# Kernel optimization log

Measured on AMD Instinct MI355X. Metric: run time of the kernel, lower is better.

Reference implementation:

```python
import jax, jax.numpy as jnp
import numpy as np

N_CLASSES = 18

def setup_inputs() -> dict:
    key = jax.random.key(0)
    k1, k2 = jax.random.split(key)
    B = 2_000_000
    output = jax.random.normal(k1, (B, N_CLASSES), dtype=jnp.float32)
    labels_soft = jax.random.uniform(k2, (B, N_CLASSES), dtype=jnp.float32)
    return {"output": output, "labels_soft": labels_soft}

def reference(output, labels_soft):
    # Original: sum over classes of mean_b( CE(output, cls) * labels_soft[:, cls] )
    # = mean over batch of sum_c( -log_softmax(output)[b, c] * labels_soft[b, c] )
    logp = jax.nn.log_softmax(output, axis=-1)          # [B, C]
    per_row = -jnp.sum(logp * labels_soft, axis=-1)     # [B]
    return jnp.mean(per_row)
```

## Files before the change

kernel.cpp:

```cpp
#include <hip/hip_runtime.h>

#define NCLS   18
#define TROWS  128
#define TWORDS (TROWS * NCLS)
#define CHUNKS (TWORDS / 256)

#define AS1 __attribute__((address_space(1)))
#define AS3 __attribute__((address_space(3)))

__global__ __launch_bounds__(256) void ce_soft_main(
    const float* __restrict__ logits,
    const float* __restrict__ labels,
    float* __restrict__ partial,
    int B)
{
    __shared__ float sX[2][TWORDS];
    __shared__ float sL[2][TWORDS];
    __shared__ float sWS[4];

    const int tid  = threadIdx.x;
    const int lane = tid & 63;
    const int wid  = tid >> 6;
    const int p    = tid >> 1;
    const int h    = tid & 1;
    const int nTiles = B / TROWS;
    const int grid = gridDim.x;

    float acc = 0.0f;
    int cur = 0;

    int t0 = blockIdx.x;
    if (t0 < nTiles) {
        const float* gx = logits + (size_t)t0 * TWORDS;
        const float* gl = labels + (size_t)t0 * TWORDS;
        for (int c = wid; c < CHUNKS; c += 4) {
            __builtin_amdgcn_global_load_lds((const AS1 void*)(gx + c * 256 + lane * 4),
                                             (AS3 void*)(&sX[0][c * 256]), 16, 0, 0);
            __builtin_amdgcn_global_load_lds((const AS1 void*)(gl + c * 256 + lane * 4),
                                             (AS3 void*)(&sL[0][c * 256]), 16, 0, 0);
        }
    }

    for (int t = t0; t < nTiles; t += grid) {
        __syncthreads();

        int tn = t + grid;
        if (tn < nTiles) {
            const float* gx = logits + (size_t)tn * TWORDS;
            const float* gl = labels + (size_t)tn * TWORDS;
            float* dX = &sX[cur ^ 1][0];
            float* dL = &sL[cur ^ 1][0];
            for (int c = wid; c < CHUNKS; c += 4) {
                __builtin_amdgcn_global_load_lds((const AS1 void*)(gx + c * 256 + lane * 4),
                                                 (AS3 void*)(dX + c * 256), 16, 0, 0);
                __builtin_amdgcn_global_load_lds((const AS1 void*)(gl + c * 256 + lane * 4),
                                                 (AS3 void*)(dL + c * 256), 16, 0, 0);
            }
        }

        const float2* rx = (const float2*)(&sX[cur][p * NCLS]);
        const float2* rl = (const float2*)(&sL[cur][p * NCLS]);
        float2 xv[5], lv[5];
        const int n = 5 - h;
        #pragma unroll
        for (int k = 0; k < 5; ++k) {
            int c = 2 * k + h;
            if (k < n) { xv[k] = rx[c];                      lv[k] = rl[c]; }
            else       { xv[k] = make_float2(-1e30f, -1e30f); lv[k] = make_float2(0.f, 0.f); }
        }
        float m = xv[0].x;
        #pragma unroll
        for (int k = 0; k < 5; ++k) { m = fmaxf(m, xv[k].x); m = fmaxf(m, xv[k].y); }
        m = fmaxf(m, __shfl_xor(m, 1, 64));
        float se = 0.f, dot = 0.f, sl = 0.f;
        #pragma unroll
        for (int k = 0; k < 5; ++k) {
            se += __expf(xv[k].x - m) + __expf(xv[k].y - m);
            dot = fmaf(lv[k].x, xv[k].x, dot);
            dot = fmaf(lv[k].y, xv[k].y, dot);
            sl += lv[k].x + lv[k].y;
        }
        se += __shfl_xor(se, 1, 64);
        float lse = m + __logf(se);
        acc = fmaf(sl, lse, acc - dot);
        cur ^= 1;
    }

    for (int row = nTiles * TROWS + blockIdx.x * blockDim.x + tid; row < B;
         row += grid * blockDim.x) {
        const float2* o2 = (const float2*)(logits + (size_t)row * NCLS);
        const float2* l2 = (const float2*)(labels + (size_t)row * NCLS);
        float x[NCLS], l[NCLS];
        #pragma unroll
        for (int k = 0; k < NCLS / 2; ++k) {
            float2 v = o2[k]; x[2 * k] = v.x; x[2 * k + 1] = v.y;
            float2 w = l2[k]; l[2 * k] = w.x; l[2 * k + 1] = w.y;
        }
        float mm = x[0];
        #pragma unroll
        for (int c = 1; c < NCLS; ++c) mm = fmaxf(mm, x[c]);
        float se = 0.f, dot = 0.f, sl = 0.f;
        #pragma unroll
        for (int c = 0; c < NCLS; ++c) {
            se += __expf(x[c] - mm);
            dot = fmaf(l[c], x[c], dot);
            sl += l[c];
        }
        acc = fmaf(sl, mm + __logf(se), acc - dot);
    }

    #pragma unroll
    for (int off = 32; off > 0; off >>= 1)
        acc += __shfl_down(acc, off, 64);
    if (lane == 0) sWS[wid] = acc;
    __syncthreads();
    if (tid == 0)
        partial[blockIdx.x] = sWS[0] + sWS[1] + sWS[2] + sWS[3];
}

__global__ __launch_bounds__(256) void ce_soft_finish(
    const float* __restrict__ partial, float* __restrict__ result,
    int n, float invB)
{
    float s = 0.f;
    for (int i = threadIdx.x; i < n; i += 256) s += partial[i];
    #pragma unroll
    for (int off = 32; off > 0; off >>= 1)
        s += __shfl_down(s, off, 64);
    __shared__ float ws[4];
    int lane = threadIdx.x & 63, wid = threadIdx.x >> 6;
    if (lane == 0) ws[wid] = s;
    __syncthreads();
    if (threadIdx.x == 0)
        result[0] = (ws[0] + ws[1] + ws[2] + ws[3]) * invB;
}

extern "C" void kernel_launch(void* const* d_in, const int* in_sizes, int n_in,
                              void* d_out, int out_size, void* d_ws, size_t ws_size,
                              hipStream_t stream) {
    const float* logits = (const float*)d_in[0];
    const float* labels = (const float*)d_in[1];
    float* result = (float*)d_out;

    int B = in_sizes[0] / NCLS;

    int grid = 1024;
    size_t need = (size_t)grid * sizeof(float);
    if (ws_size < need) {
        grid = (int)(ws_size / sizeof(float));
        if (grid > 1024) grid = 1024;
        if (grid < 1) grid = 1;
    }
    float* partial = (float*)d_ws;

    ce_soft_main<<<grid, 256, 0, stream>>>(logits, labels, partial, B);
    ce_soft_finish<<<1, 256, 0, stream>>>(partial, result, grid, 1.0f / (float)B);
}
```

Before: 286.7 us.

## Give each wave its own tiles with register double-buffered prefetch through private LDS

Replaces the block-wide LDS double buffer, which used async global-to-LDS loads and a __syncthreads every tile, with a per-wave scheme. Each wave owns its own LDS slice and keeps two tiles of logits and labels in registers, so the next loads are issued before the current tile is computed. Each lane now handles two full rows from LDS, so the pairwise shuffles go away, and the dot product is folded into a single fma per element. The grid is halved to 512 blocks with launch_bounds(256,2). The cost is very high register pressure (four 9-float4 arrays) and larger LDS per block, which may limit occupancy or cause spills.

```diff
diff --git a/kernel.cpp b/kernel.cpp
--- a/kernel.cpp
+++ b/kernel.cpp
@@ -3,91 +3,115 @@
 #define NCLS   18
 #define TROWS  128
 #define TWORDS (TROWS * NCLS)
-#define CHUNKS (TWORDS / 256)
+#define NV4    9
 
-#define AS1 __attribute__((address_space(1)))
-#define AS3 __attribute__((address_space(3)))
+__device__ __forceinline__ void tile_body(
+    float4* __restrict__ bufX, float4* __restrict__ bufL, int lane,
+    float4 (&xr)[NV4], float4 (&lr)[NV4],
+    const float* __restrict__ logits, const float* __restrict__ labels,
+    int tn, int nTiles, float& acc)
+{
+    #pragma unroll
+    for (int j = 0; j < NV4; ++j) bufX[j * 64 + lane] = xr[j];
+    #pragma unroll
+    for (int j = 0; j < NV4; ++j) bufL[j * 64 + lane] = lr[j];
 
-__global__ __launch_bounds__(256) void ce_soft_main(
+    if (tn < nTiles) {
+        const float4* gx = (const float4*)(logits + (size_t)tn * TWORDS);
+        const float4* gl = (const float4*)(labels + (size_t)tn * TWORDS);
+        #pragma unroll
+        for (int j = 0; j < NV4; ++j) xr[j] = gx[j * 64 + lane];
+        #pragma unroll
+        for (int j = 0; j < NV4; ++j) lr[j] = gl[j * 64 + lane];
+    }
+
+    float x[2 * NCLS];
+    #pragma unroll
+    for (int j = 0; j < NV4; ++j) {
+        float4 v = bufX[lane * 9 + j];
+        x[4 * j + 0] = v.x; x[4 * j + 1] = v.y;
+        x[4 * j + 2] = v.z; x[4 * j + 3] = v.w;
+    }
+    float mA = x[0], mB = x[18];
+    #pragma unroll
+    for (int c = 1; c < NCLS; ++c) { mA = fmaxf(mA, x[c]); mB = fmaxf(mB, x[NCLS + c]); }
+    float seA = 0.f, seB = 0.f;
+    #pragma unroll
+    for (int c = 0; c < NCLS; ++c) {
+        seA += __expf(x[c] - mA);
+        seB += __expf(x[NCLS + c] - mB);
+    }
+    float lseA = mA + __logf(seA);
+    float lseB = mB + __logf(seB);
+
+    #pragma unroll
+    for (int j = 0; j < NV4; ++j) {
+        float4 w = bufL[lane * 9 + j];
+        float s0 = (4 * j + 0 < NCLS) ? lseA : lseB;
+        float s1 = (4 * j + 1 < NCLS) ? lseA : lseB;
+        float s2 = (4 * j + 2 < NCLS) ? lseA : lseB;
+        float s3 = (4 * j + 3 < NCLS) ? lseA : lseB;
+        acc = fmaf(w.x, s0 - x[4 * j + 0], acc);
+        acc = fmaf(w.y, s1 - x[4 * j + 1], acc);
+        acc = fmaf(w.z, s2 - x[4 * j + 2], acc);
+        acc = fmaf(w.w, s3 - x[4 * j + 3], acc);
+    }
+}
+
+__global__ __launch_bounds__(256, 2) void ce_soft_main(
     const float* __restrict__ logits,
     const float* __restrict__ labels,
     float* __restrict__ partial,
     int B)
 {
-    __shared__ float sX[2][TWORDS];
-    __shared__ float sL[2][TWORDS];
+    __shared__ float sX[4][TWORDS];
+    __shared__ float sL[4][TWORDS];
     __shared__ float sWS[4];
 
     const int tid  = threadIdx.x;
     const int lane = tid & 63;
     const int wid  = tid >> 6;
-    const int p    = tid >> 1;
-    const int h    = tid & 1;
-    const int nTiles = B / TROWS;
-    const int grid = gridDim.x;
+    float4* bufX = (float4*)sX[wid];
+    float4* bufL = (float4*)sL[wid];
 
-    float acc = 0.0f;
-    int cur = 0;
+    const int nTiles  = B / TROWS;
+    const int wgid    = blockIdx.x * 4 + wid;
+    const int wstride = gridDim.x * 4;
 
-    int t0 = blockIdx.x;
-    if (t0 < nTiles) {
-        const float* gx = logits + (size_t)t0 * TWORDS;
-        const float* gl = labels + (size_t)t0 * TWORDS;
-        for (int c = wid; c < CHUNKS; c += 4) {
-            __builtin_amdgcn_global_load_lds((const AS1 void*)(gx + c * 256 + lane * 4),
-                                             (AS3 void*)(&sX[0][c * 256]), 16, 0, 0);
-            __builtin_amdgcn_global_load_lds((const AS1 void*)(gl + c * 256 + lane * 4),
-                                             (AS3 void*)(&sL[0][c * 256]), 16, 0, 0);
+    float acc = 0.f;
+    float4 xA[NV4], lA[NV4], xB[NV4], lB[NV4];
+
+    {
+        int tA = wgid, tB = wgid + wstride;
+        if (tA < nTiles) {
+            const float4* gx = (const float4*)(logits + (size_t)tA * TWORDS);
+            const float4* gl = (const float4*)(labels + (size_t)tA * TWORDS);
+            #pragma unroll
+            for (int j = 0; j < NV4; ++j) xA[j] = gx[j * 64 + lane];
+            #pragma unroll
+            for (int j = 0; j < NV4; ++j) lA[j] = gl[j * 64 + lane];
+        }
+        if (tB < nTiles) {
+            const float4* gx = (const float4*)(logits + (size_t)tB * TWORDS);
+            const float4* gl = (const float4*)(labels + (size_t)tB * TWORDS);
+            #pragma unroll
+            for (int j = 0; j < NV4; ++j) xB[j] = gx[j * 64 + lane];
+            #pragma unroll
+            for (int j = 0; j < NV4; ++j) lB[j] = gl[j * 64 + lane];
         }
     }
 
-    for (int t = t0; t < nTiles; t += grid) {
-        __syncthreads();
-
-        int tn = t + grid;
-        if (tn < nTiles) {
-            const float* gx = logits + (size_t)tn * TWORDS;
-            const float* gl = labels + (size_t)tn * TWORDS;
-            float* dX = &sX[cur ^ 1][0];
-            float* dL = &sL[cur ^ 1][0];
-            for (int c = wid; c < CHUNKS; c += 4) {
-                __builtin_amdgcn_global_load_lds((const AS1 void*)(gx + c * 256 + lane * 4),
-                                                 (AS3 void*)(dX + c * 256), 16, 0, 0);
-                __builtin_amdgcn_global_load_lds((const AS1 void*)(gl + c * 256 + lane * 4),
-                                                 (AS3 void*)(dL + c * 256), 16, 0, 0);
-            }
-        }
-
-        const float2* rx = (const float2*)(&sX[cur][p * NCLS]);
-        const float2* rl = (const float2*)(&sL[cur][p * NCLS]);
-        float2 xv[5], lv[5];
-        const int n = 5 - h;
-        #pragma unroll
-        for (int k = 0; k < 5; ++k) {
-            int c = 2 * k + h;
-            if (k < n) { xv[k] = rx[c];                      lv[k] = rl[c]; }
-            else       { xv[k] = make_float2(-1e30f, -1e30f); lv[k] = make_float2(0.f, 0.f); }
-        }
-        float m = xv[0].x;
-        #pragma unroll
-        for (int k = 0; k < 5; ++k) { m = fmaxf(m, xv[k].x); m = fmaxf(m, xv[k].y); }
-        m = fmaxf(m, __shfl_xor(m, 1, 64));
-        float se = 0.f, dot = 0.f, sl = 0.f;
-        #pragma unroll
-        for (int k = 0; k < 5; ++k) {
-            se += __expf(xv[k].x - m) + __expf(xv[k].y - m);
-            dot = fmaf(lv[k].x, xv[k].x, dot);
-            dot = fmaf(lv[k].y, xv[k].y, dot);
-            sl += lv[k].x + lv[k].y;
-        }
-        se += __shfl_xor(se, 1, 64);
-        float lse = m + __logf(se);
-        acc = fmaf(sl, lse, acc - dot);
-        cur ^= 1;
+    for (int t = wgid; t < nTiles; t += 2 * wstride) {
+        tile_body(bufX, bufL, lane, xA, lA, logits, labels,
+                  t + 2 * wstride, nTiles, acc);
+        int t1 = t + wstride;
+        if (t1 < nTiles)
+            tile_body(bufX, bufL, lane, xB, lB, logits, labels,
+                      t1 + 2 * wstride, nTiles, acc);
     }
 
     for (int row = nTiles * TROWS + blockIdx.x * blockDim.x + tid; row < B;
-         row += grid * blockDim.x) {
+         row += gridDim.x * blockDim.x) {
         const float2* o2 = (const float2*)(logits + (size_t)row * NCLS);
         const float2* l2 = (const float2*)(labels + (size_t)row * NCLS);
         float x[NCLS], l[NCLS];
@@ -144,11 +168,10 @@
 
     int B = in_sizes[0] / NCLS;
 
-    int grid = 1024;
-    size_t need = (size_t)grid * sizeof(float);
-    if (ws_size < need) {
+    int grid = 512;
+    if (ws_size < (size_t)grid * sizeof(float)) {
         grid = (int)(ws_size / sizeof(float));
-        if (grid > 1024) grid = 1024;
+        if (grid > 512) grid = 512;
         if (grid < 1) grid = 1;
     }
     float* partial = (float*)d_ws;
```

Result: slower. 343.2 us (+19.7%).

## Switch to per-wave tiles with register prefetch and no block barriers

Applied to the files above, without the earlier changes.

Each wavefront now processes its own 128-row tile, prefetching the next tile into registers with float4 loads and staging through a private LDS buffer, with each lane computing two full rows. This removes block-wide __syncthreads and the pairwise lane shuffles of the previous layout. The grid size is halved. It trades the async global-to-LDS double buffer for higher register pressure and possible LDS bank conflicts from the 9-float4 row stride.

```diff
diff --git a/kernel.cpp b/kernel.cpp
--- a/kernel.cpp
+++ b/kernel.cpp
@@ -3,10 +3,9 @@
 #define NCLS   18
 #define TROWS  128
 #define TWORDS (TROWS * NCLS)
-#define CHUNKS (TWORDS / 256)
+#define NF4    (TWORDS / 4)
 
-#define AS1 __attribute__((address_space(1)))
-#define AS3 __attribute__((address_space(3)))
+#define REP9(F) F(0) F(1) F(2) F(3) F(4) F(5) F(6) F(7) F(8)
 
 __global__ __launch_bounds__(256) void ce_soft_main(
     const float* __restrict__ logits,
@@ -14,80 +13,116 @@
     float* __restrict__ partial,
     int B)
 {
-    __shared__ float sX[2][TWORDS];
-    __shared__ float sL[2][TWORDS];
+    __shared__ float4 sX[4][NF4];
+    __shared__ float4 sL[4][NF4];
     __shared__ float sWS[4];
 
     const int tid  = threadIdx.x;
     const int lane = tid & 63;
     const int wid  = tid >> 6;
-    const int p    = tid >> 1;
-    const int h    = tid & 1;
-    const int nTiles = B / TROWS;
-    const int grid = gridDim.x;
+    float4* bufX = &sX[wid][0];
+    float4* bufL = &sL[wid][0];
+
+    const int nTiles  = B / TROWS;
+    const int wgid    = blockIdx.x * 4 + wid;
+    const int wstride = gridDim.x * 4;
 
     float acc = 0.0f;
-    int cur = 0;
 
-    int t0 = blockIdx.x;
-    if (t0 < nTiles) {
-        const float* gx = logits + (size_t)t0 * TWORDS;
-        const float* gl = labels + (size_t)t0 * TWORDS;
-        for (int c = wid; c < CHUNKS; c += 4) {
-            __builtin_amdgcn_global_load_lds((const AS1 void*)(gx + c * 256 + lane * 4),
-                                             (AS3 void*)(&sX[0][c * 256]), 16, 0, 0);
-            __builtin_amdgcn_global_load_lds((const AS1 void*)(gl + c * 256 + lane * 4),
-                                             (AS3 void*)(&sL[0][c * 256]), 16, 0, 0);
+#define DECLP(i) float4 px##i, pl##i;
+    REP9(DECLP)
+#undef DECLP
+
+    if (wgid < nTiles) {
+        const float4* gx = (const float4*)(logits + (size_t)wgid * TWORDS) + lane;
+        const float4* gl = (const float4*)(labels + (size_t)wgid * TWORDS) + lane;
+#define LOADP(i) px##i = gx[64 * i]; pl##i = gl[64 * i];
+        REP9(LOADP)
+#undef LOADP
+    }
+
+    for (int t = wgid; t < nTiles; t += wstride) {
+#define STX(i) bufX[64 * i + lane] = px##i;
+        REP9(STX)
+#undef STX
+#define STL(i) bufL[64 * i + lane] = pl##i;
+        REP9(STL)
+#undef STL
+
+        int tn = t + wstride;
+        if (tn < nTiles) {
+            const float4* gx = (const float4*)(logits + (size_t)tn * TWORDS) + lane;
+            const float4* gl = (const float4*)(labels + (size_t)tn * TWORDS) + lane;
+#define LOADP(i) px##i = gx[64 * i]; pl##i = gl[64 * i];
+            REP9(LOADP)
+#undef LOADP
+        }
+
+        const float4* rx = bufX + lane * 9;
+#define RDX(i) float4 v##i = rx[i];
+        REP9(RDX)
+#undef RDX
+
+        float mA = fmaxf(fmaxf(fmaxf(v0.x, v0.y), fmaxf(v0.z, v0.w)),
+                   fmaxf(fmaxf(fmaxf(v1.x, v1.y), fmaxf(v1.z, v1.w)),
+                   fmaxf(fmaxf(fmaxf(v2.x, v2.y), fmaxf(v2.z, v2.w)),
+                   fmaxf(fmaxf(fmaxf(v3.x, v3.y), fmaxf(v3.z, v3.w)),
+                         fmaxf(v4.x, v4.y)))));
+        float mB = fmaxf(fmaxf(fmaxf(v5.x, v5.y), fmaxf(v5.z, v5.w)),
+                   fmaxf(fmaxf(fmaxf(v6.x, v6.y), fmaxf(v6.z, v6.w)),
+                   fmaxf(fmaxf(fmaxf(v7.x, v7.y), fmaxf(v7.z, v7.w)),
+                   fmaxf(fmaxf(fmaxf(v8.x, v8.y), fmaxf(v8.z, v8.w)),
+                         fmaxf(v4.z, v4.w)))));
+
+        float seA = __expf(v0.x - mA) + __expf(v0.y - mA) + __expf(v0.z - mA) + __expf(v0.w - mA)
+                  + __expf(v1.x - mA) + __expf(v1.y - mA) + __expf(v1.z - mA) + __expf(v1.w - mA)
+                  + __expf(v2.x - mA) + __expf(v2.y - mA) + __expf(v2.z - mA) + __expf(v2.w - mA)
+                  + __expf(v3.x - mA) + __expf(v3.y - mA) + __expf(v3.z - mA) + __expf(v3.w - mA)
+                  + __expf(v4.x - mA) + __expf(v4.y - mA);
+        float seB = __expf(v4.z - mB) + __expf(v4.w - mB)
+                  + __expf(v5.x - mB) + __expf(v5.y - mB) + __expf(v5.z - mB) + __expf(v5.w - mB)
+                  + __expf(v6.x - mB) + __expf(v6.y - mB) + __expf(v6.z - mB) + __expf(v6.w - mB)
+                  + __expf(v7.x - mB) + __expf(v7.y - mB) + __expf(v7.z - mB) + __expf(v7.w - mB)
+                  + __expf(v8.x - mB) + __expf(v8.y - mB) + __expf(v8.z - mB) + __expf(v8.w - mB);
+
+        float lseA = mA + __logf(seA);
+        float lseB = mB + __logf(seB);
+
+        const float4* rl = bufL + lane * 9;
+        {
+            float4 w;
+            w = rl[0];
+            acc = fmaf(w.x, lseA - v0.x, acc); acc = fmaf(w.y, lseA - v0.y, acc);
+            acc = fmaf(w.z, lseA - v0.z, acc); acc = fmaf(w.w, lseA - v0.w, acc);
+            w = rl[1];
+            acc = fmaf(w.x, lseA - v1.x, acc); acc = fmaf(w.y, lseA - v1.y, acc);
+            acc = fmaf(w.z, lseA - v1.z, acc); acc = fmaf(w.w, lseA - v1.w, acc);
+            w = rl[2];
+            acc = fmaf(w.x, lseA - v2.x, acc); acc = fmaf(w.y, lseA - v2.y, acc);
+            acc = fmaf(w.z, lseA - v2.z, acc); acc = fmaf(w.w, lseA - v2.w, acc);
+            w = rl[3];
+            acc = fmaf(w.x, lseA - v3.x, acc); acc = fmaf(w.y, lseA - v3.y, acc);
+            acc = fmaf(w.z, lseA - v3.z, acc); acc = fmaf(w.w, lseA - v3.w, acc);
+            w = rl[4];
+            acc = fmaf(w.x, lseA - v4.x, acc); acc = fmaf(w.y, lseA - v4.y, acc);
+            acc = fmaf(w.z, lseB - v4.z, acc); acc = fmaf(w.w, lseB - v4.w, acc);
+            w = rl[5];
+            acc = fmaf(w.x, lseB - v5.x, acc); acc = fmaf(w.y, lseB - v5.y, acc);
+            acc = fmaf(w.z, lseB - v5.z, acc); acc = fmaf(w.w, lseB - v5.w, acc);
+            w = rl[6];
+            acc = fmaf(w.x, lseB - v6.x, acc); acc = fmaf(w.y, lseB - v6.y, acc);
+            acc = fmaf(w.z, lseB - v6.z, acc); acc = fmaf(w.w, lseB - v6.w, acc);
+            w = rl[7];
+            acc = fmaf(w.x, lseB - v7.x, acc); acc = fmaf(w.y, lseB - v7.y, acc);
+            acc = fmaf(w.z, lseB - v7.z, acc); acc = fmaf(w.w, lseB - v7.w, acc);
+            w = rl[8];
+            acc = fmaf(w.x, lseB - v8.x, acc); acc = fmaf(w.y, lseB - v8.y, acc);
+            acc = fmaf(w.z, lseB - v8.z, acc); acc = fmaf(w.w, lseB - v8.w, acc);
         }
     }
 
-    for (int t = t0; t < nTiles; t += grid) {
-        __syncthreads();
-
-        int tn = t + grid;
-        if (tn < nTiles) {
-            const float* gx = logits + (size_t)tn * TWORDS;
-            const float* gl = labels + (size_t)tn * TWORDS;
-            float* dX = &sX[cur ^ 1][0];
-            float* dL = &sL[cur ^ 1][0];
-            for (int c = wid; c < CHUNKS; c += 4) {
-                __builtin_amdgcn_global_load_lds((const AS1 void*)(gx + c * 256 + lane * 4),
-                                                 (AS3 void*)(dX + c * 256), 16, 0, 0);
-                __builtin_amdgcn_global_load_lds((const AS1 void*)(gl + c * 256 + lane * 4),
-                                                 (AS3 void*)(dL + c * 256), 16, 0, 0);
-            }
-        }
-
-        const float2* rx = (const float2*)(&sX[cur][p * NCLS]);
-        const float2* rl = (const float2*)(&sL[cur][p * NCLS]);
-        float2 xv[5], lv[5];
-        const int n = 5 - h;
-        #pragma unroll
-        for (int k = 0; k < 5; ++k) {
-            int c = 2 * k + h;
-            if (k < n) { xv[k] = rx[c];                      lv[k] = rl[c]; }
-            else       { xv[k] = make_float2(-1e30f, -1e30f); lv[k] = make_float2(0.f, 0.f); }
-        }
-        float m = xv[0].x;
-        #pragma unroll
-        for (int k = 0; k < 5; ++k) { m = fmaxf(m, xv[k].x); m = fmaxf(m, xv[k].y); }
-        m = fmaxf(m, __shfl_xor(m, 1, 64));
-        float se = 0.f, dot = 0.f, sl = 0.f;
-        #pragma unroll
-        for (int k = 0; k < 5; ++k) {
-            se += __expf(xv[k].x - m) + __expf(xv[k].y - m);
-            dot = fmaf(lv[k].x, xv[k].x, dot);
-            dot = fmaf(lv[k].y, xv[k].y, dot);
-            sl += lv[k].x + lv[k].y;
-        }
-        se += __shfl_xor(se, 1, 64);
-        float lse = m + __logf(se);
-        acc = fmaf(sl, lse, acc - dot);
-        cur ^= 1;
-    }
-
     for (int row = nTiles * TROWS + blockIdx.x * blockDim.x + tid; row < B;
-         row += grid * blockDim.x) {
+         row += gridDim.x * blockDim.x) {
         const float2* o2 = (const float2*)(logits + (size_t)row * NCLS);
         const float2* l2 = (const float2*)(labels + (size_t)row * NCLS);
         float x[NCLS], l[NCLS];
@@ -144,11 +179,10 @@
 
     int B = in_sizes[0] / NCLS;
 
-    int grid = 1024;
-    size_t need = (size_t)grid * sizeof(float);
-    if (ws_size < need) {
+    int grid = 512;
+    if (ws_size < (size_t)grid * sizeof(float)) {
         grid = (int)(ws_size / sizeof(float));
-        if (grid > 1024) grid = 1024;
+        if (grid > 512) grid = 512;
         if (grid < 1) grid = 1;
     }
     float* partial = (float*)d_ws;
```

Result: slower. 295.9 us (+3.2%).
